# Kernel optimization log

Hardware: AMD Instinct MI355X
Metric: run time of the kernel (lower is better)

Reference implementation:

```python
import jax, jax.numpy as jnp
import numpy as np

B, S, HID = 2, 2048, 2048
N_HEADS, N_KV, HD = 32, 8, 64
ROPE_BASE = 10000.0


def setup_inputs() -> dict:
    key = jax.random.key(0)
    k1, k2, k3 = jax.random.split(key, 3)
    hidden_states = jax.random.normal(k1, (B, S, HID), dtype=jnp.float32)
    position_ids = jnp.broadcast_to(jnp.arange(S, dtype=jnp.int32), (B, S))
    # additive causal mask [B, 1, S, S]
    causal = jnp.where(jnp.tril(jnp.ones((S, S), dtype=bool)), 0.0, -1e9).astype(jnp.float32)
    attention_mask = jnp.broadcast_to(causal[None, None], (B, 1, S, S))
    qkv_w = jax.random.normal(k2, (HID, N_HEADS * HD + 2 * N_KV * HD), dtype=jnp.float32) * 0.02
    o_w = jax.random.normal(k3, (HID, HID), dtype=jnp.float32) * 0.02
    return {"hidden_states": hidden_states, "position_ids": position_ids,
            "attention_mask": attention_mask, "qkv_w": qkv_w, "o_w": o_w}


def _rotate_half(x):
    x1, x2 = jnp.split(x, 2, axis=-1)
    return jnp.concatenate([-x2, x1], axis=-1)


def reference(hidden_states, position_ids, attention_mask, qkv_w, o_w):
    b, s, _ = hidden_states.shape
    qkv = hidden_states @ qkv_w  # [B,S,3072]
    q_pos = N_HEADS * HD
    kv_pos = N_KV * HD
    q = qkv[..., :q_pos].reshape(b, s, N_HEADS, HD).transpose(0, 2, 1, 3)       # [B,H,S,D]
    k = qkv[..., q_pos:q_pos + kv_pos].reshape(b, s, N_KV, HD).transpose(0, 2, 1, 3)  # [B,Hkv,S,D]
    v = qkv[..., q_pos + kv_pos:].reshape(b, s, N_KV, HD).transpose(0, 2, 1, 3)       # [B,Hkv,S,D]

    # rotary embedding (TFPhi3RotaryEmbedding)
    inv_freq = 1.0 / (ROPE_BASE ** (jnp.arange(0, HD, 2, dtype=jnp.float32) / HD))  # [D/2]
    freqs = position_ids.astype(jnp.float32)[:, :, None] * inv_freq[None, None, :]  # [B,S,D/2]
    emb = jnp.concatenate([freqs, freqs], axis=-1)  # [B,S,D]
    cos = jnp.cos(emb)[:, None]  # [B,1,S,D]
    sin = jnp.sin(emb)[:, None]
    q = q * cos + _rotate_half(q) * sin
    k = k * cos + _rotate_half(k) * sin

    # GQA: repeat_kv with n_rep = 4 (repeat_interleave over head dim)
    n_rep = N_HEADS // N_KV
    k = jnp.repeat(k, n_rep, axis=1)  # [B,H,S,D]
    v = jnp.repeat(v, n_rep, axis=1)

    scores = jnp.einsum('bhqd,bhkd->bhqk', q, k) / np.sqrt(HD).astype(np.float32)
    scores = scores + attention_mask
    weights = jax.nn.softmax(scores, axis=-1)
    attn = jnp.einsum('bhqk,bhkd->bhqd', weights, v)  # [B,H,S,D]
    attn = attn.transpose(0, 2, 1, 3).reshape(b, s, HID)
    return attn @ o_w
```

## Files before the change

kernel.cpp:

```cpp
#include <hip/hip_runtime.h>
#include <stdint.h>


typedef unsigned short u16;
typedef __bf16 bf16x8 __attribute__((ext_vector_type(8)));
typedef float f32x4 __attribute__((ext_vector_type(4)));
typedef unsigned short u16x8 __attribute__((ext_vector_type(8)));

__device__ __forceinline__ u16 f2bf(float f) {
  unsigned int u = __float_as_uint(f);
  u += 0x7fffu + ((u >> 16) & 1u);
  return (u16)(u >> 16);
}

__device__ __forceinline__ unsigned cvt_pk_bf16(float lo, float hi) {
  unsigned r;
  asm("v_cvt_pk_bf16_f32 %0, %1, %2" : "=v"(r) : "v"(lo), "v"(hi));
  return r;
}

__device__ __forceinline__ float fexp2(float x) {
  float r;
  asm("v_exp_f32 %0, %1" : "=v"(r) : "v"(x));
  return r;
}

__device__ __forceinline__ void gload_lds16(const void* g, void* l) {
  __builtin_amdgcn_global_load_lds((const __attribute__((address_space(1))) void*)g,
                                   (__attribute__((address_space(3))) void*)l, 16, 0, 0);
}

__global__ __launch_bounds__(256) void conv_bf16_kernel(const float* __restrict__ in,
                                                        u16* __restrict__ out, int n8) {
  int i = blockIdx.x * 256 + threadIdx.x;
  int stride = gridDim.x * 256;
  for (; i < n8; i += stride) {
    const float4* p = (const float4*)in + (size_t)i * 2;
    float4 a = p[0], b = p[1];
    u16x8 o;
    o[0] = f2bf(a.x); o[1] = f2bf(a.y); o[2] = f2bf(a.z); o[3] = f2bf(a.w);
    o[4] = f2bf(b.x); o[5] = f2bf(b.y); o[6] = f2bf(b.z); o[7] = f2bf(b.w);
    *(u16x8*)(out + (size_t)i * 8) = o;
  }
}

__global__ __launch_bounds__(256) void wtrans_kernel(const float* __restrict__ in,
                                                     u16* __restrict__ out, int R, int C) {
  __shared__ float tile[32][33];
  int tx = threadIdx.x & 31, ty = threadIdx.x >> 5;
  int col = blockIdx.x * 32 + tx;
  for (int j = ty; j < 32; j += 8)
    tile[j][tx] = in[(size_t)(blockIdx.y * 32 + j) * C + col];
  __syncthreads();
  int ocol = blockIdx.y * 32 + tx;
  for (int j = ty; j < 32; j += 8)
    out[(size_t)(blockIdx.x * 32 + j) * R + ocol] = f2bf(tile[tx][j]);
}

__global__ __launch_bounds__(256) void rope_table_kernel(float* __restrict__ cost,
                                                         float* __restrict__ sint) {
  int idx = blockIdx.x * 256 + threadIdx.x;
  if (idx >= 2048 * 32) return;
  int p = idx >> 5, i = idx & 31;
  float invf = powf(10000.f, -(float)i / 32.f);
  float ang = (float)p * invf;
  cost[idx] = cosf(ang);
  sint[idx] = sinf(ang);
}

__global__ __launch_bounds__(512) void gemm256_kernel(const u16* __restrict__ A,
                                                      const u16* __restrict__ Bt,
                                                      float* __restrict__ C,
                                                      int M, int N, int K) {
  __shared__ __align__(16) char lds[131072];
  const int tid = threadIdx.x;
  const int lane = tid & 63;
  const int w = tid >> 6;
  const int wm = w >> 2, wn = w & 3;

  const int nwg = gridDim.x * gridDim.y;
  const int flat = blockIdx.y * gridDim.x + blockIdx.x;
  const int cpx = nwg >> 3;
  const int swb = (flat & 7) * cpx + (flat >> 3);
  const int bx = swb % gridDim.x, by = swb / gridDim.x;
  const int brow = by * 256, bcol = bx * 256;

  const int nt = K >> 6;
  f32x4 acc[8][4] = {};

  auto stage_tile = [&](int kt, int buf) {
    char* ab = lds + buf * 65536;
    char* bb = ab + 32768;
#pragma unroll
    for (int hf = 0; hf < 2; ++hf)
#pragma unroll
      for (int i = 0; i < 2; ++i) {
        int P = (w * 2 + i) * 1024 + lane * 16;
        int L = P ^ (((P >> 9) & 1) << 5);
        int r = L >> 7, c = (L & 127) >> 1;
        gload_lds16(A + (size_t)(brow + hf * 128 + r) * K + kt + c,
                    ab + hf * 16384 + (w * 2 + i) * 1024);
      }
#pragma unroll
    for (int hf = 0; hf < 2; ++hf)
#pragma unroll
      for (int i = 0; i < 2; ++i) {
        int P = (w * 2 + i) * 1024 + lane * 16;
        int L = P ^ (((P >> 9) & 1) << 5);
        int r = L >> 7, c = (L & 127) >> 1;
        gload_lds16(Bt + (size_t)(bcol + hf * 128 + r) * K + kt + c,
                    bb + hf * 16384 + (w * 2 + i) * 1024);
      }
  };

  stage_tile(0, 0);

  for (int t = 0; t < nt; ++t) {
    const int cur = t & 1;
    const char* ah = lds + cur * 65536 + wm * 16384;
    const char* bh = lds + cur * 65536 + 32768 + (wn >> 1) * 16384;
    const int rb = (wn & 1) * 64;

    if (t + 1 < nt) {
      stage_tile((t + 1) << 6, cur ^ 1);
      asm volatile("s_waitcnt vmcnt(8)" ::: "memory");
    } else {
      asm volatile("s_waitcnt vmcnt(0)" ::: "memory");
    }
    __builtin_amdgcn_s_barrier();
    asm volatile("" ::: "memory");

#pragma unroll
    for (int p = 0; p < 4; ++p) {
      bf16x8 af[2][2], bfr[4][2];
#pragma unroll
      for (int i = 0; i < 2; ++i)
#pragma unroll
        for (int kk = 0; kk < 2; ++kk) {
          int lin = ((p * 2 + i) * 16 + (lane & 15)) * 128 + kk * 64 + (lane >> 4) * 16;
          af[i][kk] = *(const bf16x8*)(ah + (lin ^ (((lin >> 9) & 1) << 5)));
        }
#pragma unroll
      for (int fn = 0; fn < 4; ++fn)
#pragma unroll
        for (int kk = 0; kk < 2; ++kk) {
          int lin = (rb + fn * 16 + (lane & 15)) * 128 + kk * 64 + (lane >> 4) * 16;
          bfr[fn][kk] = *(const bf16x8*)(bh + (lin ^ (((lin >> 9) & 1) << 5)));
        }
      __builtin_amdgcn_s_barrier();
      __builtin_amdgcn_s_setprio(1);
#pragma unroll
      for (int i = 0; i < 2; ++i)
#pragma unroll
        for (int fn = 0; fn < 4; ++fn)
#pragma unroll
          for (int kk = 0; kk < 2; ++kk)
            acc[p * 2 + i][fn] = __builtin_amdgcn_mfma_f32_16x16x32_bf16(
                af[i][kk], bfr[fn][kk], acc[p * 2 + i][fn], 0, 0, 0);
      __builtin_amdgcn_s_setprio(0);
      __builtin_amdgcn_s_barrier();
    }
  }

#pragma unroll
  for (int fm = 0; fm < 8; ++fm) {
    int row0 = brow + wm * 128 + fm * 16 + (lane >> 4) * 4;
#pragma unroll
    for (int fn = 0; fn < 4; ++fn) {
      int col = bcol + wn * 64 + fn * 16 + (lane & 15);
#pragma unroll
      for (int j = 0; j < 4; ++j)
        C[(size_t)(row0 + j) * N + col] = acc[fm][fn][j];
    }
  }
}

__global__ __launch_bounds__(256) void rope_scatter_kernel(const float* __restrict__ qkv,
                                                           const int* __restrict__ pos_ids,
                                                           const float* __restrict__ cost,
                                                           const float* __restrict__ sint,
                                                           u16* __restrict__ Qo,
                                                           u16* __restrict__ Ko) {
  int t = blockIdx.x;
  int b = t >> 11, s = t & 2047;
  int pos = pos_ids[t];
  const float* row = qkv + (size_t)t * 3072;
  int tid = threadIdx.x;
  const float QSCALE = 0.125f * 1.44269504088896340736f;

  for (int idx = tid; idx < 1024; idx += 256) {
    int hh = idx >> 5, i = idx & 31;
    float x1 = row[hh * 64 + i], x2 = row[hh * 64 + i + 32];
    float c = cost[pos * 32 + i], sn = sint[pos * 32 + i];
    float o1 = (x1 * c - x2 * sn) * QSCALE;
    float o2 = (x2 * c + x1 * sn) * QSCALE;
    size_t base = ((size_t)(b * 32 + hh) * 2048 + s) * 64;
    Qo[base + i] = f2bf(o1);
    Qo[base + i + 32] = f2bf(o2);
  }
  {
    int hh = tid >> 5, i = tid & 31;
    float x1 = row[2048 + hh * 64 + i], x2 = row[2048 + hh * 64 + i + 32];
    float c = cost[pos * 32 + i], sn = sint[pos * 32 + i];
    float o1 = x1 * c - x2 * sn;
    float o2 = x2 * c + x1 * sn;
    size_t base = ((size_t)(b * 8 + hh) * 2048 + s) * 64;
    Ko[base + i] = f2bf(o1);
    Ko[base + i + 32] = f2bf(o2);
  }
}

__global__ __launch_bounds__(256) void vtrans_kernel(const float* __restrict__ qkv,
                                                     u16* __restrict__ Vt) {
  __shared__ float tile[64][65];
  int b = blockIdx.x >> 3, hv = blockIdx.x & 7;
  int s0 = blockIdx.y * 64;
  int tid = threadIdx.x;
  for (int idx = tid; idx < 4096; idx += 256) {
    int tok = idx >> 6, c = idx & 63;
    tile[tok][c] = qkv[(size_t)(b * 2048 + s0 + tok) * 3072 + 2560 + hv * 64 + c];
  }
  __syncthreads();
  size_t obase = (size_t)(b * 8 + hv) * 64 * 2048;
  for (int idx = tid; idx < 4096; idx += 256) {
    int d = idx >> 6, si = idx & 63;
    Vt[obase + (size_t)d * 2048 + s0 + si] = f2bf(tile[si][d]);
  }
}

__global__ __launch_bounds__(256) void attn_kernel(const u16* __restrict__ Q,
                                                   const u16* __restrict__ Kk,
                                                   const u16* __restrict__ Vt,
                                                   u16* __restrict__ O) {
  __shared__ __align__(16) u16 lds_k[2][64 * 64];
  __shared__ __align__(16) u16 lds_v[2][64 * 64];
  __shared__ __align__(16) u16 lds_p[4][1024];

  const int tid = threadIdx.x;
  const int lane = tid & 63;
  const int w = tid >> 6;
  const int g = lane >> 4;
  const int q = lane & 15;
  const int bh = blockIdx.x;
  const int b = bh >> 5, h = bh & 31, hkv = (bh & 31) >> 2;
  const size_t qbase = (size_t)(b * 32 + h) * 2048 * 64;
  const size_t kbase = (size_t)(b * 8 + hkv) * 2048 * 64;
  const size_t vbase = (size_t)(b * 8 + hkv) * 64 * 2048;
  const int pair = blockIdx.y;
  const int srcQ = (lane & 48) | (4 * g);

  auto stageKV = [&](int k0, int buf) {
#pragma unroll
    for (int i = 0; i < 2; ++i) {
      int off = w * 2048 + i * 1024 + lane * 16;
      int sw2 = off ^ (((off >> 7) & 7) << 4);
      int r = sw2 >> 7, ce = (sw2 & 127) >> 1;
      gload_lds16(Kk + kbase + (size_t)(k0 + r) * 64 + ce,
                  (u16*)lds_k[buf] + ((w * 2048 + i * 1024) >> 1));
      gload_lds16(Vt + vbase + (size_t)r * 2048 + k0 + ce,
                  (u16*)lds_v[buf] + ((w * 2048 + i * 1024) >> 1));
    }
  };

  for (int half = 0; half < 2; ++half) {
    const int qt = half ? (31 - pair) : pair;
    const int qb = qt * 64;

    bf16x8 aq[2];
    {
      const u16* qp = Q + qbase + (size_t)(qb + w * 16 + q) * 64 + g * 8;
      aq[0] = *(const bf16x8*)(qp);
      aq[1] = *(const bf16x8*)(qp + 32);
    }

    f32x4 oacc[4] = {};
    float m = -1e30f, l = 0.f;

    stageKV(0, 0);

    for (int kt = 0; kt <= qt; ++kt) {
      const int cur = kt & 1;
      if (kt < qt) {
        stageKV((kt + 1) * 64, cur ^ 1);
        asm volatile("s_waitcnt vmcnt(4)" ::: "memory");
      } else {
        asm volatile("s_waitcnt vmcnt(0)" ::: "memory");
      }
      __builtin_amdgcn_s_barrier();
      asm volatile("" ::: "memory");

      const bool diag = (kt == qt);
      const int nmax = diag ? w : 3;

      f32x4 sacc[4] = {};
#pragma unroll
      for (int n = 0; n < 4; ++n) {
        if (n > nmax) break;
        int row = n * 16 + q;
#pragma unroll
        for (int c = 0; c < 2; ++c) {
          int byte = row * 128 + c * 64 + g * 16;
          byte ^= ((row & 7) << 4);
          bf16x8 ak = *(const bf16x8*)&lds_k[cur][byte >> 1];
          sacc[n] = __builtin_amdgcn_mfma_f32_16x16x32_bf16(ak, aq[c], sacc[n], 0, 0, 0);
        }
      }

      if (diag) {
#pragma unroll
        for (int n = 0; n < 4; ++n)
#pragma unroll
          for (int j = 0; j < 4; ++j)
            if (n * 16 + 4 * g + j > w * 16 + q) sacc[n][j] = -1e30f;
      }

      float mx = sacc[0][0];
#pragma unroll
      for (int n = 0; n < 4; ++n)
#pragma unroll
        for (int j = 0; j < 4; ++j) mx = fmaxf(mx, sacc[n][j]);
      mx = fmaxf(mx, __shfl_xor(mx, 16, 64));
      mx = fmaxf(mx, __shfl_xor(mx, 32, 64));
      float mnew = fmaxf(m, mx);
      float alpha = fexp2(m - mnew);
      m = mnew;

      float p[4][4];
      float rs = 0.f;
#pragma unroll
      for (int n = 0; n < 4; ++n)
#pragma unroll
        for (int j = 0; j < 4; ++j) {
          float pv = fexp2(sacc[n][j] - mnew);
          p[n][j] = pv;
          rs += pv;
        }
      rs += __shfl_xor(rs, 16, 64);
      rs += __shfl_xor(rs, 32, 64);
      l = l * alpha + rs;

#pragma unroll
      for (int j = 0; j < 4; ++j) {
        float aj = __shfl(alpha, srcQ + j, 64);
#pragma unroll
        for (int n = 0; n < 4; ++n) oacc[n][j] *= aj;
      }

      unsigned pk[4][2];
#pragma unroll
      for (int n = 0; n < 4; ++n) {
        pk[n][0] = cvt_pk_bf16(p[n][0], p[n][1]);
        pk[n][1] = cvt_pk_bf16(p[n][2], p[n][3]);
      }
      {
        char* pbase = (char*)lds_p[w] + q * 128;
#pragma unroll
        for (int n = 0; n < 4; ++n) {
          unsigned long long v =
              (unsigned long long)pk[n][0] | ((unsigned long long)pk[n][1] << 32);
          *(unsigned long long*)(pbase + (((2 * n + (g >> 1)) ^ (q & 7)) << 4) +
                                 ((g & 1) << 3)) = v;
        }
      }

#pragma unroll
      for (int c = 0; c < 2; ++c) {
        if (diag && w < 2 && c == 1) break;
        bf16x8 pa = *(const bf16x8*)((char*)lds_p[w] + q * 128 +
                                     (((4 * c + g) ^ (q & 7)) << 4));
#pragma unroll
        for (int n = 0; n < 4; ++n) {
          int row = n * 16 + q;
          int byte = row * 128 + c * 64 + g * 16;
          byte ^= ((row & 7) << 4);
          bf16x8 bv = *(const bf16x8*)&lds_v[cur][byte >> 1];
          oacc[n] = __builtin_amdgcn_mfma_f32_16x16x32_bf16(pa, bv, oacc[n], 0, 0, 0);
        }
      }
      __builtin_amdgcn_s_barrier();
    }

    float linv[4];
#pragma unroll
    for (int j = 0; j < 4; ++j)
      linv[j] = __builtin_amdgcn_rcpf(__shfl(l, srcQ + j, 64));
#pragma unroll
    for (int n = 0; n < 4; ++n) {
      int col = h * 64 + n * 16 + q;
#pragma unroll
      for (int j = 0; j < 4; ++j) {
        int qrow = qb + w * 16 + 4 * g + j;
        O[(size_t)(b * 2048 + qrow) * 2048 + col] = f2bf(oacc[n][j] * linv[j]);
      }
    }
  }
}

extern "C" void kernel_launch(void* const* d_in, const int* in_sizes, int n_in,
                              void* d_out, int out_size, void* d_ws, size_t ws_size,
                              hipStream_t stream) {
  const float* hidden = (const float*)d_in[0];
  const int* pos = (const int*)d_in[1];
  const float* qkv_w = (const float*)d_in[3];
  const float* o_w = (const float*)d_in[4];
  float* out = (float*)d_out;
  char* ws = (char*)d_ws;

  u16* wqkvT  = (u16*)(ws + 0);
  u16* woT    = (u16*)(ws + 12582912);
  u16* hidb   = (u16*)(ws + 20971520);
  float* qkvbuf = (float*)(ws + 37748736);
  u16* kb     = (u16*)(ws + 88080384);
  u16* vtb    = (u16*)(ws + 92274688);
  float* cost = (float*)(ws + 96468992);
  float* sint = (float*)(ws + 96731136);
  u16* qbuf   = hidb;
  u16* attnb  = (u16*)qkvbuf;

  conv_bf16_kernel<<<4096, 256, 0, stream>>>(hidden, hidb, 1048576);
  wtrans_kernel<<<dim3(96, 64), 256, 0, stream>>>(qkv_w, wqkvT, 2048, 3072);
  wtrans_kernel<<<dim3(64, 64), 256, 0, stream>>>(o_w, woT, 2048, 2048);
  rope_table_kernel<<<256, 256, 0, stream>>>(cost, sint);

  gemm256_kernel<<<dim3(12, 16), 512, 0, stream>>>(hidb, wqkvT, qkvbuf, 4096, 3072, 2048);

  rope_scatter_kernel<<<4096, 256, 0, stream>>>(qkvbuf, pos, cost, sint, qbuf, kb);
  vtrans_kernel<<<dim3(16, 32), 256, 0, stream>>>(qkvbuf, vtb);

  attn_kernel<<<dim3(64, 16), 256, 0, stream>>>(qbuf, kb, vtb, attnb);

  gemm256_kernel<<<dim3(8, 16), 512, 0, stream>>>(attnb, woT, out, 4096, 2048, 2048);
}
```

Baseline: 431.0 us.

## Shrink GEMM tile to 256x128 to fill more CUs and restructure prefetch

Changes the bf16 MFMA GEMM block tile from 256x256 to 256x128, with the 8 waves laid out 4x2 and each holding 4x4 accumulator fragments. This doubles the grid for both the QKV and output projections so more of the chip's CUs get work. The LDS swizzle becomes a per-row XOR, and the next-tile global-to-LDS loads are now issued after the first k-slice fragment reads, with a full vmcnt wait at the end of each tile. The trade-off is lower arithmetic intensity per block and more redundant A-tile loads.

```diff
diff --git a/kernel.cpp b/kernel.cpp
--- a/kernel.cpp
+++ b/kernel.cpp
@@ -72,102 +72,99 @@
                                                       const u16* __restrict__ Bt,
                                                       float* __restrict__ C,
                                                       int M, int N, int K) {
-  __shared__ __align__(16) char lds[131072];
+  __shared__ __align__(16) char lds[98304];
   const int tid = threadIdx.x;
   const int lane = tid & 63;
   const int w = tid >> 6;
-  const int wm = w >> 2, wn = w & 3;
+  const int wm = w >> 1, wn = w & 1;
+  const int g = lane >> 4, lq = lane & 15;
 
   const int nwg = gridDim.x * gridDim.y;
   const int flat = blockIdx.y * gridDim.x + blockIdx.x;
   const int cpx = nwg >> 3;
   const int swb = (flat & 7) * cpx + (flat >> 3);
   const int bx = swb % gridDim.x, by = swb / gridDim.x;
-  const int brow = by * 256, bcol = bx * 256;
+  const int brow = by * 256, bcol = bx * 128;
+
+  f32x4 acc[4][4] = {};
+
+  auto stageA = [&](int kt, int buf) {
+    char* ab = lds + buf * 49152;
+#pragma unroll
+    for (int i = 0; i < 4; ++i) {
+      int D = (w * 4 + i) * 1024 + lane * 16;
+      int r = D >> 7;
+      int L = D ^ ((r & 7) << 4);
+      int ce = (L & 127) >> 1;
+      gload_lds16(A + (size_t)(brow + r) * K + kt + ce, ab + D);
+    }
+  };
+  auto stageB = [&](int kt, int buf) {
+    char* bb = lds + buf * 49152 + 32768;
+#pragma unroll
+    for (int i = 0; i < 2; ++i) {
+      int D = (w * 2 + i) * 1024 + lane * 16;
+      int r = D >> 7;
+      int L = D ^ ((r & 7) << 4);
+      int ce = (L & 127) >> 1;
+      gload_lds16(Bt + (size_t)(bcol + r) * K + kt + ce, bb + D);
+    }
+  };
+
+  stageA(0, 0);
+  stageB(0, 0);
+  asm volatile("s_waitcnt vmcnt(0)" ::: "memory");
+  __builtin_amdgcn_s_barrier();
+  asm volatile("" ::: "memory");
 
   const int nt = K >> 6;
-  f32x4 acc[8][4] = {};
-
-  auto stage_tile = [&](int kt, int buf) {
-    char* ab = lds + buf * 65536;
-    char* bb = ab + 32768;
-#pragma unroll
-    for (int hf = 0; hf < 2; ++hf)
-#pragma unroll
-      for (int i = 0; i < 2; ++i) {
-        int P = (w * 2 + i) * 1024 + lane * 16;
-        int L = P ^ (((P >> 9) & 1) << 5);
-        int r = L >> 7, c = (L & 127) >> 1;
-        gload_lds16(A + (size_t)(brow + hf * 128 + r) * K + kt + c,
-                    ab + hf * 16384 + (w * 2 + i) * 1024);
-      }
-#pragma unroll
-    for (int hf = 0; hf < 2; ++hf)
-#pragma unroll
-      for (int i = 0; i < 2; ++i) {
-        int P = (w * 2 + i) * 1024 + lane * 16;
-        int L = P ^ (((P >> 9) & 1) << 5);
-        int r = L >> 7, c = (L & 127) >> 1;
-        gload_lds16(Bt + (size_t)(bcol + hf * 128 + r) * K + kt + c,
-                    bb + hf * 16384 + (w * 2 + i) * 1024);
-      }
-  };
-
-  stage_tile(0, 0);
-
   for (int t = 0; t < nt; ++t) {
     const int cur = t & 1;
-    const char* ah = lds + cur * 65536 + wm * 16384;
-    const char* bh = lds + cur * 65536 + 32768 + (wn >> 1) * 16384;
-    const int rb = (wn & 1) * 64;
-
-    if (t + 1 < nt) {
-      stage_tile((t + 1) << 6, cur ^ 1);
-      asm volatile("s_waitcnt vmcnt(8)" ::: "memory");
-    } else {
-      asm volatile("s_waitcnt vmcnt(0)" ::: "memory");
-    }
-    __builtin_amdgcn_s_barrier();
-    asm volatile("" ::: "memory");
-
-#pragma unroll
-    for (int p = 0; p < 4; ++p) {
-      bf16x8 af[2][2], bfr[4][2];
-#pragma unroll
-      for (int i = 0; i < 2; ++i)
-#pragma unroll
-        for (int kk = 0; kk < 2; ++kk) {
-          int lin = ((p * 2 + i) * 16 + (lane & 15)) * 128 + kk * 64 + (lane >> 4) * 16;
-          af[i][kk] = *(const bf16x8*)(ah + (lin ^ (((lin >> 9) & 1) << 5)));
-        }
-#pragma unroll
-      for (int fn = 0; fn < 4; ++fn)
-#pragma unroll
-        for (int kk = 0; kk < 2; ++kk) {
-          int lin = (rb + fn * 16 + (lane & 15)) * 128 + kk * 64 + (lane >> 4) * 16;
-          bfr[fn][kk] = *(const bf16x8*)(bh + (lin ^ (((lin >> 9) & 1) << 5)));
-        }
+    const char* ab = lds + cur * 49152;
+    const char* bb = ab + 32768;
+
+#pragma unroll
+    for (int kk = 0; kk < 2; ++kk) {
+      bf16x8 af[4], bfr[4];
+#pragma unroll
+      for (int fm = 0; fm < 4; ++fm) {
+        int r = wm * 64 + fm * 16 + lq;
+        int lin = r * 128 + kk * 64 + g * 16;
+        af[fm] = *(const bf16x8*)(ab + (lin ^ ((r & 7) << 4)));
+      }
+#pragma unroll
+      for (int fn = 0; fn < 4; ++fn) {
+        int r = wn * 64 + fn * 16 + lq;
+        int lin = r * 128 + kk * 64 + g * 16;
+        bfr[fn] = *(const bf16x8*)(bb + (lin ^ ((r & 7) << 4)));
+      }
+      if (kk == 0 && t + 1 < nt) {
+        stageA((t + 1) << 6, cur ^ 1);
+        stageB((t + 1) << 6, cur ^ 1);
+      }
       __builtin_amdgcn_s_barrier();
+      asm volatile("" ::: "memory");
       __builtin_amdgcn_s_setprio(1);
 #pragma unroll
-      for (int i = 0; i < 2; ++i)
+      for (int fm = 0; fm < 4; ++fm)
 #pragma unroll
         for (int fn = 0; fn < 4; ++fn)
-#pragma unroll
-          for (int kk = 0; kk < 2; ++kk)
-            acc[p * 2 + i][fn] = __builtin_amdgcn_mfma_f32_16x16x32_bf16(
-                af[i][kk], bfr[fn][kk], acc[p * 2 + i][fn], 0, 0, 0);
+          acc[fm][fn] = __builtin_amdgcn_mfma_f32_16x16x32_bf16(
+              af[fm], bfr[fn], acc[fm][fn], 0, 0, 0);
       __builtin_amdgcn_s_setprio(0);
+      if (kk == 1 && t + 1 < nt)
+        asm volatile("s_waitcnt vmcnt(0)" ::: "memory");
       __builtin_amdgcn_s_barrier();
-    }
-  }
-
-#pragma unroll
-  for (int fm = 0; fm < 8; ++fm) {
-    int row0 = brow + wm * 128 + fm * 16 + (lane >> 4) * 4;
+      asm volatile("" ::: "memory");
+    }
+  }
+
+#pragma unroll
+  for (int fm = 0; fm < 4; ++fm) {
+    int row0 = brow + wm * 64 + fm * 16 + g * 4;
 #pragma unroll
     for (int fn = 0; fn < 4; ++fn) {
-      int col = bcol + wn * 64 + fn * 16 + (lane & 15);
+      int col = bcol + wn * 64 + fn * 16 + lq;
 #pragma unroll
       for (int j = 0; j < 4; ++j)
         C[(size_t)(row0 + j) * N + col] = acc[fm][fn][j];
@@ -422,12 +419,12 @@
   wtrans_kernel<<<dim3(64, 64), 256, 0, stream>>>(o_w, woT, 2048, 2048);
   rope_table_kernel<<<256, 256, 0, stream>>>(cost, sint);
 
-  gemm256_kernel<<<dim3(12, 16), 512, 0, stream>>>(hidb, wqkvT, qkvbuf, 4096, 3072, 2048);
+  gemm256_kernel<<<dim3(24, 16), 512, 0, stream>>>(hidb, wqkvT, qkvbuf, 4096, 3072, 2048);
 
   rope_scatter_kernel<<<4096, 256, 0, stream>>>(qkvbuf, pos, cost, sint, qbuf, kb);
   vtrans_kernel<<<dim3(16, 32), 256, 0, stream>>>(qkvbuf, vtb);
 
   attn_kernel<<<dim3(64, 16), 256, 0, stream>>>(qbuf, kb, vtb, attnb);
 
-  gemm256_kernel<<<dim3(8, 16), 512, 0, stream>>>(attnb, woT, out, 4096, 2048, 2048);
-}
+  gemm256_kernel<<<dim3(16, 16), 512, 0, stream>>>(attnb, woT, out, 4096, 2048, 2048);
+}
```

Result: faster. 357.6 us (-17.0%).
